# Kernel tuning notes

Hardware: AMD Instinct MI355X
Metric: run time of the kernel (lower is better)

The kernel has to match this reference:

```python
import jax, jax.numpy as jnp
import numpy as np

B, N, M, C = 8, 76725, 32, 12  # N = 9 anchors x (80^2+40^2+20^2+10^2+5^2) for a 640x640 image, P3-P7
IMG = 640.0


def setup_inputs() -> dict:
    key = jax.random.key(0)
    ks = jax.random.split(key, 7)
    # logits biased toward prior_prob~0.01 like the head's bias init
    cls_logits = jax.random.normal(ks[0], (B, N, C), jnp.float32) - 4.0
    box_deltas = 0.1 * jax.random.normal(ks[1], (B, N, 4), jnp.float32)
    # plausible anchors: random centers in image, sizes 16..256
    a_xy = jax.random.uniform(ks[2], (N, 2), jnp.float32) * IMG
    a_wh = 16.0 + jax.random.uniform(ks[3], (N, 2), jnp.float32) * 240.0
    anchors = jnp.concatenate([a_xy - 0.5 * a_wh, a_xy + 0.5 * a_wh], axis=-1)
    # padded ground truth: M boxes per image, all valid
    g_xy = jax.random.uniform(ks[4], (B, M, 2), jnp.float32) * (IMG - 96.0)
    g_wh = 16.0 + jax.random.uniform(ks[5], (B, M, 2), jnp.float32) * 80.0
    gt_boxes = jnp.concatenate([g_xy, g_xy + g_wh], axis=-1)
    gt_labels = jax.random.randint(ks[6], (B, M), 0, C)
    gt_valid = jnp.ones((B, M), dtype=bool)
    return {"cls_logits": cls_logits, "box_deltas": box_deltas, "anchors": anchors,
            "gt_boxes": gt_boxes, "gt_labels": gt_labels, "gt_valid": gt_valid}


def _box_iou(anchors, gt_boxes):
    # anchors [N,4], gt_boxes [B,M,4] -> [B,N,M]
    ax1, ay1, ax2, ay2 = (anchors[:, i] for i in range(4))
    gx1, gy1, gx2, gy2 = (gt_boxes[..., i] for i in range(4))
    iw = jnp.clip(jnp.minimum(ax2[None, :, None], gx2[:, None, :])
                  - jnp.maximum(ax1[None, :, None], gx1[:, None, :]), 0.0)
    ih = jnp.clip(jnp.minimum(ay2[None, :, None], gy2[:, None, :])
                  - jnp.maximum(ay1[None, :, None], gy1[:, None, :]), 0.0)
    inter = iw * ih
    area_a = (ax2 - ax1) * (ay2 - ay1)            # [N]
    area_g = (gx2 - gx1) * (gy2 - gy1)            # [B,M]
    union = area_a[None, :, None] + area_g[:, None, :] - inter
    return inter / union


def _encode_boxes(anchors, matched):
    aw = anchors[:, 2] - anchors[:, 0]
    ah = anchors[:, 3] - anchors[:, 1]
    acx = anchors[:, 0] + 0.5 * aw
    acy = anchors[:, 1] + 0.5 * ah
    gw = matched[..., 2] - matched[..., 0]
    gh = matched[..., 3] - matched[..., 1]
    gcx = matched[..., 0] + 0.5 * gw
    gcy = matched[..., 1] + 0.5 * gh
    return jnp.stack([(gcx - acx) / aw, (gcy - acy) / ah,
                      jnp.log(gw / aw), jnp.log(gh / ah)], axis=-1)


def reference(cls_logits, box_deltas, anchors, gt_boxes, gt_labels, gt_valid):
    # --- anchor assignment (box_iou + max over GT) ---
    ious = _box_iou(anchors, gt_boxes)                       # [B,N,M]
    ious = jnp.where(gt_valid[:, None, :], ious, -1.0)
    iou_max = ious.max(axis=-1)                              # [B,N]
    idx = ious.argmax(axis=-1)                               # [B,N]
    pos = iou_max >= 0.5
    valid = pos | (iou_max < 0.4)                            # non-ignore anchors
    matched = jnp.take_along_axis(
        gt_boxes, jnp.broadcast_to(idx[:, :, None], (B, N, 4)), axis=1)  # [B,N,4]
    mlab = jnp.take_along_axis(gt_labels, idx, axis=1)       # [B,N]
    f32 = cls_logits.dtype
    cls_t = jax.nn.one_hot(mlab, C, dtype=f32) * pos[..., None].astype(f32)
    # --- sigmoid focal loss (alpha=0.25, gamma=2), mean over non-ignored elements ---
    p = jax.nn.sigmoid(cls_logits)
    ce = -(cls_t * jax.nn.log_sigmoid(cls_logits)
           + (1.0 - cls_t) * jax.nn.log_sigmoid(-cls_logits))
    pt = cls_t * p + (1.0 - cls_t) * (1.0 - p)
    alpha_t = cls_t * 0.25 + (1.0 - cls_t) * 0.75
    focal = alpha_t * (1.0 - pt) ** 2 * ce                   # [B,N,C]
    vw = valid.astype(f32)
    cls_loss = jnp.sum(focal * vw[..., None]) / jnp.maximum(jnp.sum(vw) * C, 1.0)
    # --- smooth L1 (beta=1) on positives, mean over selected elements ---
    box_t = _encode_boxes(anchors, matched)                  # [B,N,4]
    d = jnp.abs(box_deltas - box_t)
    sl1 = jnp.where(d < 1.0, 0.5 * d * d, d - 0.5)
    pw = pos.astype(f32)
    box_loss = jnp.sum(sl1 * pw[..., None]) / jnp.maximum(jnp.sum(pw) * 4.0, 1.0)
    return cls_loss + box_loss
```

## Files before the change

kernel.cpp:

```cpp
#include <hip/hip_runtime.h>
#include <math.h>

#define NB 8
#define NA 76725
#define NM 32
#define NC 12
#define BLK 256
#define GX  128
#define NBLOCKS (GX * NB)


__global__ __launch_bounds__(BLK) void retina_fused(
    const float* __restrict__ cls_logits,
    const float* __restrict__ box_deltas,
    const float* __restrict__ anchors,
    const float* __restrict__ gt_boxes,
    const int* __restrict__ gt_labels,
    char* __restrict__ ws,
    int nslots, int slot_stride,
    unsigned int* __restrict__ cnt,
    float* __restrict__ out)
{
    __shared__ float4 s_gt[NM];
    __shared__ float  s_area[NM];
    __shared__ int    s_lab[NM];
    __shared__ int    s_islast;
    __shared__ double s_acc[64][4];

    const int b   = blockIdx.y;
    const int tid = threadIdx.x;

    if (tid < NM) {
        float4 g = ((const float4*)gt_boxes)[b * NM + tid];
        s_gt[tid]   = g;
        s_area[tid] = (g.z - g.x) * (g.w - g.y);
        s_lab[tid]  = gt_labels[b * NM + tid];
    }
    __syncthreads();

    float fsum = 0.0f;
    float ssum = 0.0f;
    int   vcnt = 0;
    int   pcnt = 0;

    for (int n0 = blockIdx.x * BLK; n0 < NA; n0 += GX * BLK) {
        const int n = n0 + tid;
        if (n >= NA) break;

        const float4 a = ((const float4*)anchors)[n];
        const float area_a = (a.z - a.x) * (a.w - a.y);

        float b_inter, b_uni;
        int   bidx = 0;
        {
            const float4 g = s_gt[0];
            const float iw = fmaxf(fminf(a.z, g.z) - fmaxf(a.x, g.x), 0.0f);
            const float ih = fmaxf(fminf(a.w, g.w) - fmaxf(a.y, g.y), 0.0f);
            b_inter = iw * ih;
            b_uni   = (area_a + s_area[0]) - b_inter;
        }
        #pragma unroll
        for (int m = 1; m < NM; ++m) {
            const float4 g = s_gt[m];
            const float iw = fmaxf(fminf(a.z, g.z) - fmaxf(a.x, g.x), 0.0f);
            const float ih = fmaxf(fminf(a.w, g.w) - fmaxf(a.y, g.y), 0.0f);
            const float inter = iw * ih;
            const float uni   = (area_a + s_area[m]) - inter;
            const bool gt = inter * b_uni > b_inter * uni;
            b_inter = gt ? inter : b_inter;
            b_uni   = gt ? uni   : b_uni;
            bidx    = gt ? m     : bidx;
        }

        const bool pos   = (b_inter >= 0.5f * b_uni);
        const bool valid = pos || (b_inter < 0.4f * b_uni);
        vcnt += valid ? 1 : 0;
        pcnt += pos ? 1 : 0;

        if (valid) {
            const int lab = pos ? s_lab[bidx] : -1;
            const float4* cl =
                (const float4*)(cls_logits + ((size_t)b * NA + n) * NC);
            float x[NC];
            const float4 c0 = cl[0], c1 = cl[1], c2 = cl[2];
            x[0]=c0.x; x[1]=c0.y; x[2]=c0.z; x[3]=c0.w;
            x[4]=c1.x; x[5]=c1.y; x[6]=c1.z; x[7]=c1.w;
            x[8]=c2.x; x[9]=c2.y; x[10]=c2.z; x[11]=c2.w;
            #pragma unroll
            for (int c = 0; c < NC; ++c) {
                const float xx = x[c];
                const float ax = fabsf(xx);
                const float e  = __expf(-ax);
                const float t  = 1.0f + e;
                const float l1pe = __logf(t);
                const float u  = __builtin_amdgcn_rcpf(t);
                const float v  = e * u;
                const bool xpos = (xx >= 0.0f);
                const float sp_mx = l1pe + fmaxf(-xx, 0.0f);
                const float sp_px = l1pe + fmaxf(xx, 0.0f);
                const bool tgt = (c == lab);
                const float q = tgt ? (xpos ? v : u) : (xpos ? u : v);
                const float s = tgt ? sp_mx : sp_px;
                const float al = tgt ? 0.25f : 0.75f;
                fsum += al * q * q * s;
            }
        }

        if (pos) {
            const float4 g = s_gt[bidx];
            const float aw  = a.z - a.x;
            const float ah  = a.w - a.y;
            const float r_aw = __builtin_amdgcn_rcpf(aw);
            const float r_ah = __builtin_amdgcn_rcpf(ah);
            const float acx = a.x + 0.5f * aw;
            const float acy = a.y + 0.5f * ah;
            const float gw  = g.z - g.x;
            const float gh  = g.w - g.y;
            const float gcx = g.x + 0.5f * gw;
            const float gcy = g.y + 0.5f * gh;
            const float t0 = (gcx - acx) * r_aw;
            const float t1 = (gcy - acy) * r_ah;
            const float t2 = __logf(gw * r_aw);
            const float t3 = __logf(gh * r_ah);
            const float4 d4 =
                ((const float4*)box_deltas)[(size_t)b * NA + n];
            float d;
            d = fabsf(d4.x - t0); ssum += (d < 1.0f) ? 0.5f * d * d : d - 0.5f;
            d = fabsf(d4.y - t1); ssum += (d < 1.0f) ? 0.5f * d * d : d - 0.5f;
            d = fabsf(d4.z - t2); ssum += (d < 1.0f) ? 0.5f * d * d : d - 0.5f;
            d = fabsf(d4.w - t3); ssum += (d < 1.0f) ? 0.5f * d * d : d - 0.5f;
        }
    }

    float4 v = make_float4(fsum, ssum, (float)vcnt, (float)pcnt);
    #pragma unroll
    for (int off = 32; off > 0; off >>= 1) {
        v.x += __shfl_down(v.x, off);
        v.y += __shfl_down(v.y, off);
        v.z += __shfl_down(v.z, off);
        v.w += __shfl_down(v.w, off);
    }
    __shared__ float4 s_red[BLK / 64];
    const int wave = tid >> 6;
    const int lane = tid & 63;
    if (lane == 0) s_red[wave] = v;
    __syncthreads();

    if (tid == 0) {
        float4 t = s_red[0];
        #pragma unroll
        for (int w = 1; w < BLK / 64; ++w) {
            t.x += s_red[w].x; t.y += s_red[w].y;
            t.z += s_red[w].z; t.w += s_red[w].w;
        }
        const int slot = (blockIdx.y * GX + blockIdx.x) & (nslots - 1);
        double* a = (double*)(ws + (size_t)slot * slot_stride);
        atomicAdd(&a[0], (double)t.x);
        atomicAdd(&a[1], (double)t.y);
        atomicAdd(&a[2], (double)t.z);
        atomicAdd(&a[3], (double)t.w);
        __threadfence();
        const unsigned int old = atomicAdd(cnt, 1u);
        s_islast = (old == NBLOCKS - 1) ? 1 : 0;
    }
    __syncthreads();

    if (s_islast) {
        __threadfence();
        if (tid < nslots) {
            const double* a = (const double*)(ws + (size_t)tid * slot_stride);
            #pragma unroll
            for (int j = 0; j < 4; ++j)
                s_acc[tid][j] = __hip_atomic_load(&a[j], __ATOMIC_RELAXED,
                                                  __HIP_MEMORY_SCOPE_AGENT);
        }
        __syncthreads();
        if (tid == 0) {
            double fs = 0.0, ss = 0.0, vc = 0.0, pc = 0.0;
            for (int k = 0; k < nslots; ++k) {
                fs += s_acc[k][0]; ss += s_acc[k][1];
                vc += s_acc[k][2]; pc += s_acc[k][3];
            }
            const double cls_loss = fs / fmax(vc * (double)NC, 1.0);
            const double box_loss = ss / fmax(pc * 4.0, 1.0);
            out[0] = (float)(cls_loss + box_loss);
        }
    }
}

extern "C" void kernel_launch(void* const* d_in, const int* in_sizes, int n_in,
                              void* d_out, int out_size, void* d_ws, size_t ws_size,
                              hipStream_t stream) {
    const float* cls_logits = (const float*)d_in[0];
    const float* box_deltas = (const float*)d_in[1];
    const float* anchors    = (const float*)d_in[2];
    const float* gt_boxes   = (const float*)d_in[3];
    const int*   gt_labels  = (const int*)d_in[4];
    float* out = (float*)d_out;

    int nslots, stride;
    if (ws_size >= (size_t)(64 * 64 + 8)) { nslots = 64; stride = 64; }
    else                                  { nslots = 1;  stride = 32; }
    unsigned int* cnt = (unsigned int*)((char*)d_ws + (size_t)nslots * stride);

    hipMemsetAsync(d_ws, 0, (size_t)nslots * stride + 8, stream);
    dim3 grid(GX, NB);
    retina_fused<<<grid, BLK, 0, stream>>>(
        cls_logits, box_deltas, anchors, gt_boxes, gt_labels,
        (char*)d_ws, nslots, stride, cnt, out);
}
```

Before: 122.5 us.

## Use one anchor per thread, split IoU argmax chains, and add a separate finalize kernel

Each thread now handles exactly one anchor, with a grid of 300x8 blocks instead of a grid-stride loop. All loads (anchor, logits, deltas) are issued at kernel start so they overlap the IoU work. The 32-way IoU argmax is split into four independent chains to add instruction-level parallelism. The focal and box losses are computed branch-free and masked afterwards. The atomic and last-block counter reduction is replaced by per-block partial writes, with no memset when workspace allows, plus a tiny second kernel that does the final sum, at the cost of an extra launch and unconditional loads of logits and deltas.

```diff
diff --git a/kernel.cpp b/kernel.cpp
--- a/kernel.cpp
+++ b/kernel.cpp
@@ -6,29 +6,34 @@
 #define NM 32
 #define NC 12
 #define BLK 256
-#define GX  128
-#define NBLOCKS (GX * NB)
-
-
-__global__ __launch_bounds__(BLK) void retina_fused(
+#define CHX 300
+#define NBLOCKS (CHX * NB)
+
+
+__global__ __launch_bounds__(BLK, 4) void retina_main(
     const float* __restrict__ cls_logits,
     const float* __restrict__ box_deltas,
     const float* __restrict__ anchors,
     const float* __restrict__ gt_boxes,
     const int* __restrict__ gt_labels,
     char* __restrict__ ws,
-    int nslots, int slot_stride,
-    unsigned int* __restrict__ cnt,
-    float* __restrict__ out)
+    int mode, int nslots, int sstride)
 {
     __shared__ float4 s_gt[NM];
     __shared__ float  s_area[NM];
     __shared__ int    s_lab[NM];
-    __shared__ int    s_islast;
-    __shared__ double s_acc[64][4];
-
-    const int b   = blockIdx.y;
-    const int tid = threadIdx.x;
+    __shared__ float4 s_red[BLK / 64];
+
+    const int b    = blockIdx.y;
+    const int tid  = threadIdx.x;
+    const int n    = blockIdx.x * BLK + tid;
+    const bool live = (n < NA);
+    const int nc   = live ? n : (NA - 1);
+
+    const float4 a = ((const float4*)anchors)[nc];
+    const float4* clp = (const float4*)(cls_logits + ((size_t)b * NA + nc) * NC);
+    const float4 c0 = clp[0], c1 = clp[1], c2 = clp[2];
+    const float4 d4 = ((const float4*)box_deltas)[(size_t)b * NA + nc];
 
     if (tid < NM) {
         float4 g = ((const float4*)gt_boxes)[b * NM + tid];
@@ -38,112 +43,105 @@
     }
     __syncthreads();
 
-    float fsum = 0.0f;
-    float ssum = 0.0f;
-    int   vcnt = 0;
-    int   pcnt = 0;
-
-    for (int n0 = blockIdx.x * BLK; n0 < NA; n0 += GX * BLK) {
-        const int n = n0 + tid;
-        if (n >= NA) break;
-
-        const float4 a = ((const float4*)anchors)[n];
-        const float area_a = (a.z - a.x) * (a.w - a.y);
-
-        float b_inter, b_uni;
-        int   bidx = 0;
-        {
-            const float4 g = s_gt[0];
-            const float iw = fmaxf(fminf(a.z, g.z) - fmaxf(a.x, g.x), 0.0f);
-            const float ih = fmaxf(fminf(a.w, g.w) - fmaxf(a.y, g.y), 0.0f);
-            b_inter = iw * ih;
-            b_uni   = (area_a + s_area[0]) - b_inter;
-        }
+    const float area_a = (a.z - a.x) * (a.w - a.y);
+
+    float bi[4], bS[4]; int bx[4];
+    #pragma unroll
+    for (int q = 0; q < 4; ++q) {
+        const int m0 = q * 8;
+        float4 g = s_gt[m0];
+        float iw = fmaxf(fminf(a.z, g.z) - fmaxf(a.x, g.x), 0.0f);
+        float ih = fmaxf(fminf(a.w, g.w) - fmaxf(a.y, g.y), 0.0f);
+        bi[q] = iw * ih;
+        bS[q] = area_a + s_area[m0];
+        bx[q] = m0;
         #pragma unroll
-        for (int m = 1; m < NM; ++m) {
-            const float4 g = s_gt[m];
-            const float iw = fmaxf(fminf(a.z, g.z) - fmaxf(a.x, g.x), 0.0f);
-            const float ih = fmaxf(fminf(a.w, g.w) - fmaxf(a.y, g.y), 0.0f);
+        for (int mm = 1; mm < 8; ++mm) {
+            const int m = m0 + mm;
+            g  = s_gt[m];
+            iw = fmaxf(fminf(a.z, g.z) - fmaxf(a.x, g.x), 0.0f);
+            ih = fmaxf(fminf(a.w, g.w) - fmaxf(a.y, g.y), 0.0f);
             const float inter = iw * ih;
-            const float uni   = (area_a + s_area[m]) - inter;
-            const bool gt = inter * b_uni > b_inter * uni;
-            b_inter = gt ? inter : b_inter;
-            b_uni   = gt ? uni   : b_uni;
-            bidx    = gt ? m     : bidx;
-        }
-
-        const bool pos   = (b_inter >= 0.5f * b_uni);
-        const bool valid = pos || (b_inter < 0.4f * b_uni);
-        vcnt += valid ? 1 : 0;
-        pcnt += pos ? 1 : 0;
-
-        if (valid) {
-            const int lab = pos ? s_lab[bidx] : -1;
-            const float4* cl =
-                (const float4*)(cls_logits + ((size_t)b * NA + n) * NC);
-            float x[NC];
-            const float4 c0 = cl[0], c1 = cl[1], c2 = cl[2];
-            x[0]=c0.x; x[1]=c0.y; x[2]=c0.z; x[3]=c0.w;
-            x[4]=c1.x; x[5]=c1.y; x[6]=c1.z; x[7]=c1.w;
-            x[8]=c2.x; x[9]=c2.y; x[10]=c2.z; x[11]=c2.w;
-            #pragma unroll
-            for (int c = 0; c < NC; ++c) {
-                const float xx = x[c];
-                const float ax = fabsf(xx);
-                const float e  = __expf(-ax);
-                const float t  = 1.0f + e;
-                const float l1pe = __logf(t);
-                const float u  = __builtin_amdgcn_rcpf(t);
-                const float v  = e * u;
-                const bool xpos = (xx >= 0.0f);
-                const float sp_mx = l1pe + fmaxf(-xx, 0.0f);
-                const float sp_px = l1pe + fmaxf(xx, 0.0f);
-                const bool tgt = (c == lab);
-                const float q = tgt ? (xpos ? v : u) : (xpos ? u : v);
-                const float s = tgt ? sp_mx : sp_px;
-                const float al = tgt ? 0.25f : 0.75f;
-                fsum += al * q * q * s;
-            }
-        }
-
-        if (pos) {
-            const float4 g = s_gt[bidx];
-            const float aw  = a.z - a.x;
-            const float ah  = a.w - a.y;
-            const float r_aw = __builtin_amdgcn_rcpf(aw);
-            const float r_ah = __builtin_amdgcn_rcpf(ah);
-            const float acx = a.x + 0.5f * aw;
-            const float acy = a.y + 0.5f * ah;
-            const float gw  = g.z - g.x;
-            const float gh  = g.w - g.y;
-            const float gcx = g.x + 0.5f * gw;
-            const float gcy = g.y + 0.5f * gh;
-            const float t0 = (gcx - acx) * r_aw;
-            const float t1 = (gcy - acy) * r_ah;
-            const float t2 = __logf(gw * r_aw);
-            const float t3 = __logf(gh * r_ah);
-            const float4 d4 =
-                ((const float4*)box_deltas)[(size_t)b * NA + n];
-            float d;
-            d = fabsf(d4.x - t0); ssum += (d < 1.0f) ? 0.5f * d * d : d - 0.5f;
-            d = fabsf(d4.y - t1); ssum += (d < 1.0f) ? 0.5f * d * d : d - 0.5f;
-            d = fabsf(d4.z - t2); ssum += (d < 1.0f) ? 0.5f * d * d : d - 0.5f;
-            d = fabsf(d4.w - t3); ssum += (d < 1.0f) ? 0.5f * d * d : d - 0.5f;
-        }
-    }
-
-    float4 v = make_float4(fsum, ssum, (float)vcnt, (float)pcnt);
+            const float S     = area_a + s_area[m];
+            const bool gt = inter * bS[q] > bi[q] * S;
+            bi[q] = gt ? inter : bi[q];
+            bS[q] = gt ? S     : bS[q];
+            bx[q] = gt ? m     : bx[q];
+        }
+    }
+    float Bi = bi[0], BS = bS[0]; int Bx = bx[0];
+    #pragma unroll
+    for (int q = 1; q < 4; ++q) {
+        const bool gt = bi[q] * BS > Bi * bS[q];
+        Bi = gt ? bi[q] : Bi;
+        BS = gt ? bS[q] : BS;
+        Bx = gt ? bx[q] : Bx;
+    }
+    const float Bu = BS - Bi;
+
+    const bool pos   = live && (Bi >= 0.5f * Bu);
+    const bool valid = live && (pos || (Bi < 0.4f * Bu));
+
+    const int lab = pos ? s_lab[Bx] : -1;
+    float x[NC];
+    x[0]=c0.x; x[1]=c0.y; x[2]=c0.z; x[3]=c0.w;
+    x[4]=c1.x; x[5]=c1.y; x[6]=c1.z; x[7]=c1.w;
+    x[8]=c2.x; x[9]=c2.y; x[10]=c2.z; x[11]=c2.w;
+    float facc = 0.0f;
+    #pragma unroll
+    for (int c = 0; c < NC; ++c) {
+        const float xx = x[c];
+        const bool tgt = (c == lab);
+        const float z  = tgt ? -xx : xx;
+        const float e  = __expf(-fabsf(xx));
+        const float t  = 1.0f + e;
+        const float l  = __logf(t);
+        const float u  = __builtin_amdgcn_rcpf(t);
+        const float v  = e * u;
+        const float q  = (z >= 0.0f) ? u : v;
+        const float s  = l + fmaxf(z, 0.0f);
+        const float al = tgt ? 0.25f : 0.75f;
+        facc += al * (q * q) * s;
+    }
+
+    float sacc = 0.0f;
+    {
+        const float4 g  = s_gt[Bx];
+        const float aw  = a.z - a.x;
+        const float ah  = a.w - a.y;
+        const float r_aw = __builtin_amdgcn_rcpf(aw);
+        const float r_ah = __builtin_amdgcn_rcpf(ah);
+        const float acx = a.x + 0.5f * aw;
+        const float acy = a.y + 0.5f * ah;
+        const float gw  = g.z - g.x;
+        const float gh  = g.w - g.y;
+        const float gcx = g.x + 0.5f * gw;
+        const float gcy = g.y + 0.5f * gh;
+        const float t0 = (gcx - acx) * r_aw;
+        const float t1 = (gcy - acy) * r_ah;
+        const float t2 = __logf(gw * r_aw);
+        const float t3 = __logf(gh * r_ah);
+        float d;
+        d = fabsf(d4.x - t0); sacc += (d < 1.0f) ? 0.5f * d * d : d - 0.5f;
+        d = fabsf(d4.y - t1); sacc += (d < 1.0f) ? 0.5f * d * d : d - 0.5f;
+        d = fabsf(d4.z - t2); sacc += (d < 1.0f) ? 0.5f * d * d : d - 0.5f;
+        d = fabsf(d4.w - t3); sacc += (d < 1.0f) ? 0.5f * d * d : d - 0.5f;
+    }
+
+    float4 v4 = make_float4(valid ? facc : 0.0f,
+                            pos   ? sacc : 0.0f,
+                            valid ? 1.0f : 0.0f,
+                            pos   ? 1.0f : 0.0f);
     #pragma unroll
     for (int off = 32; off > 0; off >>= 1) {
-        v.x += __shfl_down(v.x, off);
-        v.y += __shfl_down(v.y, off);
-        v.z += __shfl_down(v.z, off);
-        v.w += __shfl_down(v.w, off);
-    }
-    __shared__ float4 s_red[BLK / 64];
+        v4.x += __shfl_down(v4.x, off);
+        v4.y += __shfl_down(v4.y, off);
+        v4.z += __shfl_down(v4.z, off);
+        v4.w += __shfl_down(v4.w, off);
+    }
     const int wave = tid >> 6;
     const int lane = tid & 63;
-    if (lane == 0) s_red[wave] = v;
+    if (lane == 0) s_red[wave] = v4;
     __syncthreads();
 
     if (tid == 0) {
@@ -153,38 +151,55 @@
             t.x += s_red[w].x; t.y += s_red[w].y;
             t.z += s_red[w].z; t.w += s_red[w].w;
         }
-        const int slot = (blockIdx.y * GX + blockIdx.x) & (nslots - 1);
-        double* a = (double*)(ws + (size_t)slot * slot_stride);
-        atomicAdd(&a[0], (double)t.x);
-        atomicAdd(&a[1], (double)t.y);
-        atomicAdd(&a[2], (double)t.z);
-        atomicAdd(&a[3], (double)t.w);
-        __threadfence();
-        const unsigned int old = atomicAdd(cnt, 1u);
-        s_islast = (old == NBLOCKS - 1) ? 1 : 0;
+        const int bid = blockIdx.y * gridDim.x + blockIdx.x;
+        if (mode == 2) {
+            double* p = (double*)(ws + (size_t)bid * 32);
+            p[0] = (double)t.x; p[1] = (double)t.y;
+            p[2] = (double)t.z; p[3] = (double)t.w;
+        } else {
+            double* p = (double*)(ws + (size_t)(bid & (nslots - 1)) * sstride);
+            atomicAdd(&p[0], (double)t.x);
+            atomicAdd(&p[1], (double)t.y);
+            atomicAdd(&p[2], (double)t.z);
+            atomicAdd(&p[3], (double)t.w);
+        }
+    }
+}
+
+__global__ __launch_bounds__(256) void retina_finalize(
+    const char* __restrict__ ws, int nslots, int sstride,
+    float* __restrict__ out)
+{
+    const int tid = threadIdx.x;
+    double fs = 0.0, ss = 0.0, vc = 0.0, pc = 0.0;
+    for (int i = tid; i < nslots; i += 256) {
+        const double* p = (const double*)(ws + (size_t)i * sstride);
+        fs += p[0]; ss += p[1]; vc += p[2]; pc += p[3];
+    }
+    #pragma unroll
+    for (int off = 32; off > 0; off >>= 1) {
+        fs += __shfl_down(fs, off);
+        ss += __shfl_down(ss, off);
+        vc += __shfl_down(vc, off);
+        pc += __shfl_down(pc, off);
+    }
+    __shared__ double sred[4][4];
+    const int wave = tid >> 6;
+    const int lane = tid & 63;
+    if (lane == 0) {
+        sred[wave][0] = fs; sred[wave][1] = ss;
+        sred[wave][2] = vc; sred[wave][3] = pc;
     }
     __syncthreads();
-
-    if (s_islast) {
-        __threadfence();
-        if (tid < nslots) {
-            const double* a = (const double*)(ws + (size_t)tid * slot_stride);
-            #pragma unroll
-            for (int j = 0; j < 4; ++j)
-                s_acc[tid][j] = __hip_atomic_load(&a[j], __ATOMIC_RELAXED,
-                                                  __HIP_MEMORY_SCOPE_AGENT);
-        }
-        __syncthreads();
-        if (tid == 0) {
-            double fs = 0.0, ss = 0.0, vc = 0.0, pc = 0.0;
-            for (int k = 0; k < nslots; ++k) {
-                fs += s_acc[k][0]; ss += s_acc[k][1];
-                vc += s_acc[k][2]; pc += s_acc[k][3];
-            }
-            const double cls_loss = fs / fmax(vc * (double)NC, 1.0);
-            const double box_loss = ss / fmax(pc * 4.0, 1.0);
-            out[0] = (float)(cls_loss + box_loss);
-        }
+    if (tid == 0) {
+        #pragma unroll
+        for (int w = 1; w < 4; ++w) {
+            fs += sred[w][0]; ss += sred[w][1];
+            vc += sred[w][2]; pc += sred[w][3];
+        }
+        const double cls_loss = fs / fmax(vc * (double)NC, 1.0);
+        const double box_loss = ss / fmax(pc * 4.0, 1.0);
+        out[0] = (float)(cls_loss + box_loss);
     }
 }
 
@@ -198,14 +213,17 @@
     const int*   gt_labels  = (const int*)d_in[4];
     float* out = (float*)d_out;
 
-    int nslots, stride;
-    if (ws_size >= (size_t)(64 * 64 + 8)) { nslots = 64; stride = 64; }
-    else                                  { nslots = 1;  stride = 32; }
-    unsigned int* cnt = (unsigned int*)((char*)d_ws + (size_t)nslots * stride);
-
-    hipMemsetAsync(d_ws, 0, (size_t)nslots * stride + 8, stream);
-    dim3 grid(GX, NB);
-    retina_fused<<<grid, BLK, 0, stream>>>(
+    int mode, nslots, sstride;
+    if (ws_size >= (size_t)NBLOCKS * 32)      { mode = 2; nslots = NBLOCKS; sstride = 32; }
+    else if (ws_size >= (size_t)(64 * 64))    { mode = 1; nslots = 64;      sstride = 64; }
+    else                                       { mode = 0; nslots = 1;       sstride = 32; }
+
+    if (mode != 2)
+        hipMemsetAsync(d_ws, 0, (size_t)nslots * sstride, stream);
+
+    dim3 grid(CHX, NB);
+    retina_main<<<grid, BLK, 0, stream>>>(
         cls_logits, box_deltas, anchors, gt_boxes, gt_labels,
-        (char*)d_ws, nslots, stride, cnt, out);
+        (char*)d_ws, mode, nslots, sstride);
+    retina_finalize<<<1, 256, 0, stream>>>((const char*)d_ws, nslots, sstride, out);
 }
```

Measured after the change: 101.9 us. 1.2x faster.
